# Performance work log

Hardware: AMD Instinct MI355X
Metric: run time of the kernel (lower is better)

## Reference

```python
import jax, jax.numpy as jnp
import numpy as np

T = 512          # num_frames
IN_DIM = 85      # pose+beta feature dim
HID = 1024       # hidden_dim
LAYERS = 3       # num_stacks
VERTS = 6890     # SMPL mesh vertices


def _lstm_layer(x_seq, W_ih, W_hh, b_ih, b_hh):
    """Single-layer LSTM over time, batch=1 (PyTorch gate order i,f,g,o).
    x_seq: [T, in_dim] -> hs: [T, HID]"""
    h0 = jnp.zeros((HID,), dtype=x_seq.dtype)
    c0 = jnp.zeros((HID,), dtype=x_seq.dtype)
    # precompute input contributions for all timesteps in one GEMM: [T, 4H]
    x_gates = x_seq @ W_ih.T + (b_ih + b_hh)

    def step(carry, xg):
        h, c = carry
        gates = xg + W_hh @ h          # [4H]
        i, f, g, o = jnp.split(gates, 4)
        i = jax.nn.sigmoid(i)
        f = jax.nn.sigmoid(f)
        g = jnp.tanh(g)
        o = jax.nn.sigmoid(o)
        c = f * c + i * g
        h = o * jnp.tanh(c)
        return (h, c), h

    (_, _), hs = jax.lax.scan(step, (h0, c0), x_gates)
    return hs


def setup_inputs() -> dict:
    key = jax.random.key(0)
    ks = jax.random.split(key, 4 * LAYERS + 2)
    inp = {"pose_beta_seq": jax.random.normal(ks[0], (T, IN_DIM), dtype=jnp.float32)}
    s = 1.0 / np.sqrt(HID)  # PyTorch uniform(-1/sqrt(h), 1/sqrt(h)) init scale
    ki = 1
    for l in range(LAYERS):
        in_dim = IN_DIM if l == 0 else HID
        inp[f"W_ih_{l}"] = jax.random.uniform(ks[ki + 0], (4 * HID, in_dim), minval=-s, maxval=s, dtype=jnp.float32)
        inp[f"W_hh_{l}"] = jax.random.uniform(ks[ki + 1], (4 * HID, HID), minval=-s, maxval=s, dtype=jnp.float32)
        inp[f"b_ih_{l}"] = jax.random.uniform(ks[ki + 2], (4 * HID,), minval=-s, maxval=s, dtype=jnp.float32)
        inp[f"b_hh_{l}"] = jax.random.uniform(ks[ki + 3], (4 * HID,), minval=-s, maxval=s, dtype=jnp.float32)
        ki += 4
    inp["W_out"] = jax.random.uniform(ks[ki], (VERTS * 3, HID), minval=-s, maxval=s, dtype=jnp.float32)
    return inp


def reference(pose_beta_seq, W_ih_0, W_hh_0, b_ih_0, b_hh_0,
              W_ih_1, W_hh_1, b_ih_1, b_hh_1,
              W_ih_2, W_hh_2, b_ih_2, b_hh_2, W_out):
    layers = [(W_ih_0, W_hh_0, b_ih_0, b_hh_0),
              (W_ih_1, W_hh_1, b_ih_1, b_hh_1),
              (W_ih_2, W_hh_2, b_ih_2, b_hh_2)]
    h = pose_beta_seq
    for (Wih, Whh, bih, bhh) in layers:
        h = _lstm_layer(h, Wih, Whh, bih, bhh)
    dbs = (h @ W_out.T).reshape(T, VERTS, 3)
    return dbs
```

## Files before the change

kernel.cpp:

```cpp
#include <hip/hip_runtime.h>
#include <stdint.h>

#define TT    512
#define HID   1024
#define G4    4096
#define INDIM 85
#define NOUT  20670

__global__ __launch_bounds__(256)
void gemm_nt(const float* __restrict__ A, const float* __restrict__ B,
             const float* __restrict__ bias0, const float* __restrict__ bias1,
             float* __restrict__ C, int M, int N, int K)
{
    __shared__ float As[16 * 68];
    __shared__ float Bs[16 * 68];
    const int tid = threadIdx.x;
    const int tx = tid & 15, ty = tid >> 4;
    const int m0 = blockIdx.y * 64, n0 = blockIdx.x * 64;
    float acc[4][4] = {};
    const int KT = (K + 15) >> 4;

    for (int kt = 0; kt < KT; ++kt) {
        const int k0 = kt << 4;
        __syncthreads();
        for (int l = tid; l < 1024; l += 256) {
            const int mm = l >> 4, kk = l & 15;
            const int kg = k0 + kk;
            As[kk * 68 + mm] = (kg < K) ? A[(size_t)(m0 + mm) * K + kg] : 0.f;
            Bs[kk * 68 + mm] = (kg < K && (n0 + mm) < N)
                                   ? B[(size_t)(n0 + mm) * K + kg] : 0.f;
        }
        __syncthreads();
        #pragma unroll
        for (int kk = 0; kk < 16; ++kk) {
            const float4 av = *(const float4*)&As[kk * 68 + ty * 4];
            const float4 bv = *(const float4*)&Bs[kk * 68 + tx * 4];
            const float a[4] = {av.x, av.y, av.z, av.w};
            const float b[4] = {bv.x, bv.y, bv.z, bv.w};
            #pragma unroll
            for (int i = 0; i < 4; ++i)
                #pragma unroll
                for (int j = 0; j < 4; ++j)
                    acc[i][j] += a[i] * b[j];
        }
    }

    float bj[4];
    #pragma unroll
    for (int j = 0; j < 4; ++j) {
        const int n = n0 + tx * 4 + j;
        float bv = 0.f;
        if (n < N) {
            if (bias0) bv += bias0[n];
            if (bias1) bv += bias1[n];
        }
        bj[j] = bv;
    }
    #pragma unroll
    for (int i = 0; i < 4; ++i) {
        const int m = m0 + ty * 4 + i;
        #pragma unroll
        for (int j = 0; j < 4; ++j) {
            const int n = n0 + tx * 4 + j;
            if (n < N) C[(size_t)m * N + n] = acc[i][j] + bj[j];
        }
    }
}

__device__ __forceinline__ float sig_(float x) { return 1.f / (1.f + expf(-x)); }

__global__ __launch_bounds__(256)
void lstm_scan(const float* __restrict__ xg,
               const float* __restrict__ Whh,
               unsigned long long* __restrict__ hbuf,
               float* __restrict__ hs,
               const int tagbase)
{
    __shared__ float h_lds[HID];
    __shared__ float red[4 * 64 * 5];
    const int tid = threadIdx.x;
    const int w = tid >> 6, ln = tid & 63;
    const int b = blockIdx.x;

    float Wreg[4][16];
    #pragma unroll
    for (int rr = 0; rr < 4; ++rr) {
        const float* wp = Whh + (size_t)(w * HID + 4 * b + rr) * HID;
        #pragma unroll
        for (int j = 0; j < 4; ++j) {
            const float4 v = *(const float4*)&wp[256 * j + 4 * ln];
            Wreg[rr][4 * j + 0] = v.x; Wreg[rr][4 * j + 1] = v.y;
            Wreg[rr][4 * j + 2] = v.z; Wreg[rr][4 * j + 3] = v.w;
        }
    }

    float c = 0.f;
    for (int t = 0; t < TT; ++t) {
        float xv = 0.f;
        if (w == 0 && ln < 16)
            xv = xg[(size_t)t * G4 + (ln >> 2) * HID + 4 * b + (ln & 3)];

        if (t == 0) {
            *(float4*)&h_lds[4 * tid] = make_float4(0.f, 0.f, 0.f, 0.f);
        } else {
            const unsigned long long tag = (unsigned long long)(unsigned)(tagbase + t - 1);
            unsigned long long* p = hbuf + (size_t)(t - 1) * HID + 4 * tid;
            unsigned long long v0, v1, v2, v3;
            int guard = 0;
            for (;;) {
                v0 = __hip_atomic_load(p + 0, __ATOMIC_RELAXED, __HIP_MEMORY_SCOPE_AGENT);
                v1 = __hip_atomic_load(p + 1, __ATOMIC_RELAXED, __HIP_MEMORY_SCOPE_AGENT);
                v2 = __hip_atomic_load(p + 2, __ATOMIC_RELAXED, __HIP_MEMORY_SCOPE_AGENT);
                v3 = __hip_atomic_load(p + 3, __ATOMIC_RELAXED, __HIP_MEMORY_SCOPE_AGENT);
                if ((v0 >> 32) == tag && (v1 >> 32) == tag &&
                    (v2 >> 32) == tag && (v3 >> 32) == tag) break;
                if (++guard > (1 << 22)) break;
            }
            *(float4*)&h_lds[4 * tid] = make_float4(
                __uint_as_float((unsigned)v0), __uint_as_float((unsigned)v1),
                __uint_as_float((unsigned)v2), __uint_as_float((unsigned)v3));
        }
        __syncthreads();

        float hreg[16];
        #pragma unroll
        for (int j = 0; j < 4; ++j) {
            const float4 v = *(const float4*)&h_lds[256 * j + 4 * ln];
            hreg[4 * j + 0] = v.x; hreg[4 * j + 1] = v.y;
            hreg[4 * j + 2] = v.z; hreg[4 * j + 3] = v.w;
        }
        float acc[4];
        #pragma unroll
        for (int rr = 0; rr < 4; ++rr) {
            float s = 0.f;
            #pragma unroll
            for (int q = 0; q < 16; ++q) s += Wreg[rr][q] * hreg[q];
            acc[rr] = s;
        }
        #pragma unroll
        for (int rr = 0; rr < 4; ++rr) red[(w * 64 + ln) * 5 + rr] = acc[rr];
        __syncthreads();

        if (w == 0) {
            const int rbi = ln & 15, q = ln >> 4;
            const int ws = rbi >> 2, rr = rbi & 3;
            float s = 0.f;
            #pragma unroll
            for (int l2 = 0; l2 < 16; ++l2)
                s += red[(ws * 64 + q * 16 + l2) * 5 + rr];
            s += __shfl_xor(s, 16, 64);
            s += __shfl_xor(s, 32, 64);
            const float gate = s + xv;
            const int uu = ln & 3;
            const float gi = __shfl(gate, uu, 64);
            const float gf = __shfl(gate, 4 + uu, 64);
            const float gg = __shfl(gate, 8 + uu, 64);
            const float go = __shfl(gate, 12 + uu, 64);
            if (ln < 4) {
                const float i_ = sig_(gi), f_ = sig_(gf), o_ = sig_(go);
                const float g_ = tanhf(gg);
                c = f_ * c + i_ * g_;
                const float h = o_ * tanhf(c);
                const int unit = 4 * b + ln;
                hs[(size_t)t * HID + unit] = h;
                const unsigned long long pv =
                    (((unsigned long long)(unsigned)(tagbase + t)) << 32) |
                    (unsigned long long)__float_as_uint(h);
                __hip_atomic_store(hbuf + (size_t)t * HID + unit, pv,
                                   __ATOMIC_RELAXED, __HIP_MEMORY_SCOPE_AGENT);
            }
        }
    }
}

extern "C" void kernel_launch(void* const* d_in, const int* in_sizes, int n_in,
                              void* d_out, int out_size, void* d_ws, size_t ws_size,
                              hipStream_t stream)
{
    (void)in_sizes; (void)n_in; (void)out_size; (void)ws_size;

    const float* pose = (const float*)d_in[0];
    const float* Wih[3] = {(const float*)d_in[1], (const float*)d_in[5], (const float*)d_in[9]};
    const float* Whh[3] = {(const float*)d_in[2], (const float*)d_in[6], (const float*)d_in[10]};
    const float* bih[3] = {(const float*)d_in[3], (const float*)d_in[7], (const float*)d_in[11]};
    const float* bhh[3] = {(const float*)d_in[4], (const float*)d_in[8], (const float*)d_in[12]};
    const float* Wout = (const float*)d_in[13];
    float* out = (float*)d_out;

    char* ws = (char*)d_ws;
    unsigned long long* hbuf = (unsigned long long*)ws;
    float* xg  = (float*)(ws + (size_t)TT * HID * 8);
    float* hs0 = (float*)(ws + (size_t)TT * HID * 8 + (size_t)TT * G4 * 4);
    float* hs1 = hs0 + (size_t)TT * HID;
    float* hs2 = hs1 + (size_t)TT * HID;

    hipMemsetAsync(hbuf, 0, (size_t)TT * HID * sizeof(unsigned long long), stream);

    const dim3 blk(256);
    const dim3 gX(G4 / 64, TT / 64);

    gemm_nt<<<gX, blk, 0, stream>>>(pose, Wih[0], bih[0], bhh[0], xg, TT, G4, INDIM);
    lstm_scan<<<dim3(256), blk, 0, stream>>>(xg, Whh[0], hbuf, hs0, 0 * 1024 + 1);
    gemm_nt<<<gX, blk, 0, stream>>>(hs0, Wih[1], bih[1], bhh[1], xg, TT, G4, HID);
    lstm_scan<<<dim3(256), blk, 0, stream>>>(xg, Whh[1], hbuf, hs1, 1 * 1024 + 1);
    gemm_nt<<<gX, blk, 0, stream>>>(hs1, Wih[2], bih[2], bhh[2], xg, TT, G4, HID);
    lstm_scan<<<dim3(256), blk, 0, stream>>>(xg, Whh[2], hbuf, hs2, 2 * 1024 + 1);
    gemm_nt<<<dim3((NOUT + 63) / 64, TT / 64), blk, 0, stream>>>(
        hs2, Wout, nullptr, nullptr, out, TT, NOUT, HID);
}
```

Baseline: 5.789 ms.

## Fuse three LSTM layers into one wavefront-pipelined persistent kernel

Replaces three sequential per-layer scans and the intermediate input-projection GEMMs with one kernel of 768 blocks. Layers 1 and 2 compute their input projection on the fly from register-resident W_ih, and each layer polls tagged h buffers from the layer below and from its own previous step, so the layers run as a diagonal wavefront. Each block now holds half W_ih and half W_hh in registers and reduces with wave shuffles instead of an LDS reduction. This removes two GEMMs and two serial scan phases. The cost is doubled matmul work per step, higher register pressure, and a reliance on all 768 blocks being co-resident (two per CU) to avoid deadlock.

After: 4.924 ms. 14.9% less time.

```diff
diff --git a/kernel.cpp b/kernel.cpp
--- a/kernel.cpp
+++ b/kernel.cpp
@@ -6,6 +6,8 @@
 #define G4    4096
 #define INDIM 85
 #define NOUT  20670
+
+typedef unsigned long long u64;
 
 __global__ __launch_bounds__(256)
 void gemm_nt(const float* __restrict__ A, const float* __restrict__ B,
@@ -69,104 +71,145 @@
 
 __device__ __forceinline__ float sig_(float x) { return 1.f / (1.f + expf(-x)); }
 
-__global__ __launch_bounds__(256)
-void lstm_scan(const float* __restrict__ xg,
-               const float* __restrict__ Whh,
-               unsigned long long* __restrict__ hbuf,
-               float* __restrict__ hs,
-               const int tagbase)
+__global__ __launch_bounds__(256, 2)
+void lstm_fused(const float* __restrict__ xg,
+                const float* __restrict__ Whh0,
+                const float* __restrict__ Wih1, const float* __restrict__ Whh1,
+                const float* __restrict__ bih1, const float* __restrict__ bhh1,
+                const float* __restrict__ Wih2, const float* __restrict__ Whh2,
+                const float* __restrict__ bih2, const float* __restrict__ bhh2,
+                u64* __restrict__ hbuf0, u64* __restrict__ hbuf1,
+                u64* __restrict__ hbuf2, float* __restrict__ hs2)
 {
-    __shared__ float h_lds[HID];
-    __shared__ float red[4 * 64 * 5];
+    __shared__ float hin_lds[HID];
+    __shared__ float hprev_lds[HID];
+    __shared__ float gates[4][4];
+
     const int tid = threadIdx.x;
-    const int w = tid >> 6, ln = tid & 63;
-    const int b = blockIdx.x;
-
-    float Wreg[4][16];
-    #pragma unroll
-    for (int rr = 0; rr < 4; ++rr) {
-        const float* wp = Whh + (size_t)(w * HID + 4 * b + rr) * HID;
-        #pragma unroll
-        for (int j = 0; j < 4; ++j) {
-            const float4 v = *(const float4*)&wp[256 * j + 4 * ln];
-            Wreg[rr][4 * j + 0] = v.x; Wreg[rr][4 * j + 1] = v.y;
-            Wreg[rr][4 * j + 2] = v.z; Wreg[rr][4 * j + 3] = v.w;
-        }
+    const int w = tid >> 6, ln = tid & 63, q = ln & 31;
+    const bool inHalf = (ln < 32);
+    const int layer = blockIdx.x >> 8;
+    const int b = blockIdx.x & 255;
+    const int u0 = 4 * b;
+
+    const float* Wih = (layer == 1) ? Wih1 : Wih2;
+    const float* Whh = (layer == 0) ? Whh0 : (layer == 1 ? Whh1 : Whh2);
+    u64* hbI = (layer == 1) ? hbuf0 : hbuf1;
+    u64* hbP = (layer == 0) ? hbuf0 : (layer == 1 ? hbuf1 : hbuf2);
+
+    float4 Wv[4][8];
+    if (layer == 0 && inHalf) {
+        #pragma unroll
+        for (int rr = 0; rr < 4; ++rr)
+            #pragma unroll
+            for (int j = 0; j < 8; ++j)
+                Wv[rr][j] = make_float4(0.f, 0.f, 0.f, 0.f);
+    } else {
+        const float* M = inHalf ? Wih : Whh;
+        #pragma unroll
+        for (int rr = 0; rr < 4; ++rr) {
+            const float* rp = M + (size_t)(w * HID + u0 + rr) * HID + 4 * q;
+            #pragma unroll
+            for (int j = 0; j < 8; ++j)
+                Wv[rr][j] = *(const float4*)(rp + 128 * j);
+        }
+    }
+
+    float addv = 0.f;
+    if (w == 0 && ln < 16 && layer > 0) {
+        const int r = (ln >> 2) * HID + u0 + (ln & 3);
+        addv = (layer == 1) ? (bih1[r] + bhh1[r]) : (bih2[r] + bhh2[r]);
+    }
+
+    if (layer == 0) {
+        const int p4z = 4 * ((tid + b) & 255);
+        *(float4*)&hin_lds[p4z] = make_float4(0.f, 0.f, 0.f, 0.f);
     }
 
     float c = 0.f;
     for (int t = 0; t < TT; ++t) {
-        float xv = 0.f;
-        if (w == 0 && ln < 16)
-            xv = xg[(size_t)t * G4 + (ln >> 2) * HID + 4 * b + (ln & 3)];
-
-        if (t == 0) {
-            *(float4*)&h_lds[4 * tid] = make_float4(0.f, 0.f, 0.f, 0.f);
-        } else {
-            const unsigned long long tag = (unsigned long long)(unsigned)(tagbase + t - 1);
-            unsigned long long* p = hbuf + (size_t)(t - 1) * HID + 4 * tid;
-            unsigned long long v0, v1, v2, v3;
-            int guard = 0;
-            for (;;) {
-                v0 = __hip_atomic_load(p + 0, __ATOMIC_RELAXED, __HIP_MEMORY_SCOPE_AGENT);
-                v1 = __hip_atomic_load(p + 1, __ATOMIC_RELAXED, __HIP_MEMORY_SCOPE_AGENT);
-                v2 = __hip_atomic_load(p + 2, __ATOMIC_RELAXED, __HIP_MEMORY_SCOPE_AGENT);
-                v3 = __hip_atomic_load(p + 3, __ATOMIC_RELAXED, __HIP_MEMORY_SCOPE_AGENT);
-                if ((v0 >> 32) == tag && (v1 >> 32) == tag &&
-                    (v2 >> 32) == tag && (v3 >> 32) == tag) break;
-                if (++guard > (1 << 22)) break;
+        if (layer == 0 && w == 0 && ln < 16)
+            addv = xg[(size_t)t * G4 + (ln >> 2) * HID + u0 + (ln & 3)];
+
+        const int p4 = 4 * ((tid + b) & 255);
+        bool doneP = (t == 0), doneI = (layer == 0);
+        u64 vp0 = 0, vp1 = 0, vp2 = 0, vp3 = 0;
+        u64 vi0 = 0, vi1 = 0, vi2 = 0, vi3 = 0;
+        const u64 tagP = (u64)(unsigned)t;
+        const u64 tagI = (u64)(unsigned)(t + 1);
+        const u64* pp = hbP + (size_t)(t - 1) * HID + p4;
+        const u64* pi = hbI + (size_t)t * HID + p4;
+        int guard = 0;
+        while (!(doneP && doneI)) {
+            if (!doneP) {
+                vp0 = __hip_atomic_load(pp + 0, __ATOMIC_RELAXED, __HIP_MEMORY_SCOPE_AGENT);
+                vp1 = __hip_atomic_load(pp + 1, __ATOMIC_RELAXED, __HIP_MEMORY_SCOPE_AGENT);
+                vp2 = __hip_atomic_load(pp + 2, __ATOMIC_RELAXED, __HIP_MEMORY_SCOPE_AGENT);
+                vp3 = __hip_atomic_load(pp + 3, __ATOMIC_RELAXED, __HIP_MEMORY_SCOPE_AGENT);
+                doneP = (vp0 >> 32) == tagP && (vp1 >> 32) == tagP &&
+                        (vp2 >> 32) == tagP && (vp3 >> 32) == tagP;
             }
-            *(float4*)&h_lds[4 * tid] = make_float4(
-                __uint_as_float((unsigned)v0), __uint_as_float((unsigned)v1),
-                __uint_as_float((unsigned)v2), __uint_as_float((unsigned)v3));
-        }
-        __syncthreads();
-
-        float hreg[16];
-        #pragma unroll
-        for (int j = 0; j < 4; ++j) {
-            const float4 v = *(const float4*)&h_lds[256 * j + 4 * ln];
-            hreg[4 * j + 0] = v.x; hreg[4 * j + 1] = v.y;
-            hreg[4 * j + 2] = v.z; hreg[4 * j + 3] = v.w;
-        }
-        float acc[4];
-        #pragma unroll
-        for (int rr = 0; rr < 4; ++rr) {
-            float s = 0.f;
-            #pragma unroll
-            for (int q = 0; q < 16; ++q) s += Wreg[rr][q] * hreg[q];
-            acc[rr] = s;
-        }
-        #pragma unroll
-        for (int rr = 0; rr < 4; ++rr) red[(w * 64 + ln) * 5 + rr] = acc[rr];
+            if (!doneI) {
+                vi0 = __hip_atomic_load(pi + 0, __ATOMIC_RELAXED, __HIP_MEMORY_SCOPE_AGENT);
+                vi1 = __hip_atomic_load(pi + 1, __ATOMIC_RELAXED, __HIP_MEMORY_SCOPE_AGENT);
+                vi2 = __hip_atomic_load(pi + 2, __ATOMIC_RELAXED, __HIP_MEMORY_SCOPE_AGENT);
+                vi3 = __hip_atomic_load(pi + 3, __ATOMIC_RELAXED, __HIP_MEMORY_SCOPE_AGENT);
+                doneI = (vi0 >> 32) == tagI && (vi1 >> 32) == tagI &&
+                        (vi2 >> 32) == tagI && (vi3 >> 32) == tagI;
+            }
+            if (++guard > (1 << 22)) break;
+        }
+        if (t == 0)
+            *(float4*)&hprev_lds[p4] = make_float4(0.f, 0.f, 0.f, 0.f);
+        else
+            *(float4*)&hprev_lds[p4] = make_float4(
+                __uint_as_float((unsigned)vp0), __uint_as_float((unsigned)vp1),
+                __uint_as_float((unsigned)vp2), __uint_as_float((unsigned)vp3));
+        if (layer > 0)
+            *(float4*)&hin_lds[p4] = make_float4(
+                __uint_as_float((unsigned)vi0), __uint_as_float((unsigned)vi1),
+                __uint_as_float((unsigned)vi2), __uint_as_float((unsigned)vi3));
+        __syncthreads();
+
+        const float* hsrc = inHalf ? (hin_lds + 4 * q) : (hprev_lds + 4 * q);
+        float a0 = 0.f, a1 = 0.f, a2 = 0.f, a3 = 0.f;
+        #pragma unroll
+        for (int j = 0; j < 8; ++j) {
+            const float4 hv = *(const float4*)(hsrc + 128 * j);
+            a0 += Wv[0][j].x * hv.x + Wv[0][j].y * hv.y + Wv[0][j].z * hv.z + Wv[0][j].w * hv.w;
+            a1 += Wv[1][j].x * hv.x + Wv[1][j].y * hv.y + Wv[1][j].z * hv.z + Wv[1][j].w * hv.w;
+            a2 += Wv[2][j].x * hv.x + Wv[2][j].y * hv.y + Wv[2][j].z * hv.z + Wv[2][j].w * hv.w;
+            a3 += Wv[3][j].x * hv.x + Wv[3][j].y * hv.y + Wv[3][j].z * hv.z + Wv[3][j].w * hv.w;
+        }
+        #pragma unroll
+        for (int off = 1; off < 64; off <<= 1) {
+            a0 += __shfl_xor(a0, off, 64);
+            a1 += __shfl_xor(a1, off, 64);
+            a2 += __shfl_xor(a2, off, 64);
+            a3 += __shfl_xor(a3, off, 64);
+        }
+        if (ln == 0) {
+            gates[w][0] = a0; gates[w][1] = a1; gates[w][2] = a2; gates[w][3] = a3;
+        }
         __syncthreads();
 
         if (w == 0) {
-            const int rbi = ln & 15, q = ln >> 4;
-            const int ws = rbi >> 2, rr = rbi & 3;
-            float s = 0.f;
-            #pragma unroll
-            for (int l2 = 0; l2 < 16; ++l2)
-                s += red[(ws * 64 + q * 16 + l2) * 5 + rr];
-            s += __shfl_xor(s, 16, 64);
-            s += __shfl_xor(s, 32, 64);
-            const float gate = s + xv;
             const int uu = ln & 3;
-            const float gi = __shfl(gate, uu, 64);
-            const float gf = __shfl(gate, 4 + uu, 64);
-            const float gg = __shfl(gate, 8 + uu, 64);
-            const float go = __shfl(gate, 12 + uu, 64);
+            const float xi = __shfl(addv, uu, 64);
+            const float xf = __shfl(addv, 4 + uu, 64);
+            const float xgv = __shfl(addv, 8 + uu, 64);
+            const float xo = __shfl(addv, 12 + uu, 64);
             if (ln < 4) {
-                const float i_ = sig_(gi), f_ = sig_(gf), o_ = sig_(go);
-                const float g_ = tanhf(gg);
+                const float i_ = sig_(gates[0][ln] + xi);
+                const float f_ = sig_(gates[1][ln] + xf);
+                const float g_ = tanhf(gates[2][ln] + xgv);
+                const float o_ = sig_(gates[3][ln] + xo);
                 c = f_ * c + i_ * g_;
                 const float h = o_ * tanhf(c);
-                const int unit = 4 * b + ln;
-                hs[(size_t)t * HID + unit] = h;
-                const unsigned long long pv =
-                    (((unsigned long long)(unsigned)(tagbase + t)) << 32) |
-                    (unsigned long long)__float_as_uint(h);
-                __hip_atomic_store(hbuf + (size_t)t * HID + unit, pv,
+                if (layer == 2) hs2[(size_t)t * HID + u0 + ln] = h;
+                const u64 pv = (((u64)(unsigned)(t + 1)) << 32) |
+                               (u64)__float_as_uint(h);
+                __hip_atomic_store(hbP + (size_t)t * HID + u0 + ln, pv,
                                    __ATOMIC_RELAXED, __HIP_MEMORY_SCOPE_AGENT);
             }
         }
@@ -180,31 +223,37 @@
     (void)in_sizes; (void)n_in; (void)out_size; (void)ws_size;
 
     const float* pose = (const float*)d_in[0];
-    const float* Wih[3] = {(const float*)d_in[1], (const float*)d_in[5], (const float*)d_in[9]};
-    const float* Whh[3] = {(const float*)d_in[2], (const float*)d_in[6], (const float*)d_in[10]};
-    const float* bih[3] = {(const float*)d_in[3], (const float*)d_in[7], (const float*)d_in[11]};
-    const float* bhh[3] = {(const float*)d_in[4], (const float*)d_in[8], (const float*)d_in[12]};
+    const float* Wih0 = (const float*)d_in[1];
+    const float* Whh0 = (const float*)d_in[2];
+    const float* bih0 = (const float*)d_in[3];
+    const float* bhh0 = (const float*)d_in[4];
+    const float* Wih1 = (const float*)d_in[5];
+    const float* Whh1 = (const float*)d_in[6];
+    const float* bih1 = (const float*)d_in[7];
+    const float* bhh1 = (const float*)d_in[8];
+    const float* Wih2 = (const float*)d_in[9];
+    const float* Whh2 = (const float*)d_in[10];
+    const float* bih2 = (const float*)d_in[11];
+    const float* bhh2 = (const float*)d_in[12];
     const float* Wout = (const float*)d_in[13];
     float* out = (float*)d_out;
 
     char* ws = (char*)d_ws;
-    unsigned long long* hbuf = (unsigned long long*)ws;
-    float* xg  = (float*)(ws + (size_t)TT * HID * 8);
-    float* hs0 = (float*)(ws + (size_t)TT * HID * 8 + (size_t)TT * G4 * 4);
-    float* hs1 = hs0 + (size_t)TT * HID;
-    float* hs2 = hs1 + (size_t)TT * HID;
-
-    hipMemsetAsync(hbuf, 0, (size_t)TT * HID * sizeof(unsigned long long), stream);
+    const size_t HB = (size_t)TT * HID * sizeof(u64);
+    u64* hbuf0 = (u64*)ws;
+    u64* hbuf1 = (u64*)(ws + HB);
+    u64* hbuf2 = (u64*)(ws + 2 * HB);
+    float* xg  = (float*)(ws + 3 * HB);
+    float* hs2 = (float*)(ws + 3 * HB + (size_t)TT * G4 * sizeof(float));
+
+    hipMemsetAsync(hbuf0, 0, 3 * HB, stream);
 
     const dim3 blk(256);
-    const dim3 gX(G4 / 64, TT / 64);
-
-    gemm_nt<<<gX, blk, 0, stream>>>(pose, Wih[0], bih[0], bhh[0], xg, TT, G4, INDIM);
-    lstm_scan<<<dim3(256), blk, 0, stream>>>(xg, Whh[0], hbuf, hs0, 0 * 1024 + 1);
-    gemm_nt<<<gX, blk, 0, stream>>>(hs0, Wih[1], bih[1], bhh[1], xg, TT, G4, HID);
-    lstm_scan<<<dim3(256), blk, 0, stream>>>(xg, Whh[1], hbuf, hs1, 1 * 1024 + 1);
-    gemm_nt<<<gX, blk, 0, stream>>>(hs1, Wih[2], bih[2], bhh[2], xg, TT, G4, HID);
-    lstm_scan<<<dim3(256), blk, 0, stream>>>(xg, Whh[2], hbuf, hs2, 2 * 1024 + 1);
+    gemm_nt<<<dim3(G4 / 64, TT / 64), blk, 0, stream>>>(
+        pose, Wih0, bih0, bhh0, xg, TT, G4, INDIM);
+    lstm_fused<<<dim3(768), blk, 0, stream>>>(
+        xg, Whh0, Wih1, Whh1, bih1, bhh1, Wih2, Whh2, bih2, bhh2,
+        hbuf0, hbuf1, hbuf2, hs2);
     gemm_nt<<<dim3((NOUT + 63) / 64, TT / 64), blk, 0, stream>>>(
         hs2, Wout, nullptr, nullptr, out, TT, NOUT, HID);
 }
```
